# Kernel tuning notes

Measured on AMD Instinct MI355X. Metric: run time of the kernel, lower is better.

Reference implementation:

```python
import jax, jax.numpy as jnp
import numpy as np

N_NODES = 100000
N_EDGES = 1600000
IN_G = 128
IN_R = 64
HID = 128
N_GRAPHS = 512
BN_EPS = 1e-5


def _gcn_conv(x, W, b, src, dst, norm, n_nodes):
    # PyG GCNConv: h = X W; out[i] = sum_j norm_ij * h[j] over edges (incl. self-loops); + bias
    h = x @ W  # [N, C]
    msgs = h[src] * norm[:, None]  # [E', C]
    agg = jax.ops.segment_sum(msgs, dst, num_segments=n_nodes)
    return agg + b


def setup_inputs() -> dict:
    key = jax.random.key(0)
    ks = jax.random.split(key, 12)
    x = jax.random.normal(ks[0], (N_NODES, IN_G), dtype=jnp.float32)
    edge_index = jax.random.randint(ks[1], (2, N_EDGES), 0, N_NODES, dtype=jnp.int64)
    batch = jnp.sort(jax.random.randint(ks[2], (N_NODES,), 0, N_GRAPHS, dtype=jnp.int64))
    rst = jax.random.normal(ks[3], (N_GRAPHS, IN_R), dtype=jnp.float32)

    def lin(k, fan_in, fan_out):
        bound = 1.0 / np.sqrt(fan_in)
        k1, k2 = jax.random.split(k)
        W = jax.random.uniform(k1, (fan_in, fan_out), minval=-bound, maxval=bound, dtype=jnp.float32)
        b = jax.random.uniform(k2, (fan_out,), minval=-bound, maxval=bound, dtype=jnp.float32)
        return W, b

    W1, b1 = lin(ks[4], IN_G, HID)
    W2, b2 = lin(ks[5], HID, HID)
    Wg, bg = lin(ks[6], HID, HID // 2)
    Wr, br = lin(ks[7], IN_R, HID // 2)
    Wc, bc = lin(ks[8], HID, 2)
    gamma = jnp.ones((HID,), dtype=jnp.float32)
    beta = jnp.zeros((HID,), dtype=jnp.float32)
    return {"x": x, "edge_index": edge_index, "batch": batch, "rst": rst,
            "num_graphs": N_GRAPHS,
            "W1": W1, "b1": b1, "gamma": gamma, "beta": beta,
            "W2": W2, "b2": b2, "Wg": Wg, "bg": bg,
            "Wr": Wr, "br": br, "Wc": Wc, "bc": bc}


def reference(x, edge_index, batch, rst, num_graphs,
              W1, b1, gamma, beta, W2, b2, Wg, bg, Wr, br, Wc, bc):
    n = x.shape[0]
    # add self-loops (PyG GCNConv default)
    loop = jnp.arange(n, dtype=edge_index.dtype)
    src = jnp.concatenate([edge_index[0], loop])
    dst = jnp.concatenate([edge_index[1], loop])
    deg = jax.ops.segment_sum(jnp.ones_like(dst, dtype=x.dtype), dst, num_segments=n)
    dinv = jnp.where(deg > 0, jax.lax.rsqrt(deg), 0.0)
    norm = dinv[src] * dinv[dst]  # [E+N]

    h = _gcn_conv(x, W1, b1, src, dst, norm, n)
    # BatchNorm1d with batch statistics (training math; dropout omitted / eval)
    mu = jnp.mean(h, axis=0)
    var = jnp.var(h, axis=0)
    h = gamma * (h - mu) * jax.lax.rsqrt(var + BN_EPS) + beta
    h = jax.nn.relu(h)
    h = _gcn_conv(h, W2, b2, src, dst, norm, n)

    # global mean pool
    sums = jax.ops.segment_sum(h, batch, num_segments=num_graphs)
    counts = jax.ops.segment_sum(jnp.ones((n,), dtype=h.dtype), batch, num_segments=num_graphs)
    pooled = sums / jnp.maximum(counts, 1.0)[:, None]  # [G, HID]

    x_graph = jax.nn.relu(pooled @ Wg + bg)
    x_rst = jax.nn.relu(rst @ Wr + br)
    x_comb = jnp.concatenate([x_graph, x_rst], axis=1)
    return x_comb @ Wc + bc
```

## Files before the change

kernel.cpp:

```cpp
#include <hip/hip_runtime.h>


typedef __attribute__((ext_vector_type(8))) short bf16x8;
typedef __attribute__((ext_vector_type(4))) float f32x4;
typedef __attribute__((ext_vector_type(2))) float f32x2;
typedef __attribute__((ext_vector_type(2))) unsigned u32x2;
typedef __attribute__((ext_vector_type(4))) unsigned u32x4;

#define NBKT_MAX 256
#define BKT_SHIFT 9
#define TILE_E 2000
#define BSORT_CAP 4096

__device__ __forceinline__ float bf_lo(unsigned u) {
  union { unsigned u; float f; } c; c.u = u << 16; return c.f;
}
__device__ __forceinline__ float bf_hi(unsigned u) {
  union { unsigned u; float f; } c; c.u = u & 0xffff0000u; return c.f;
}
__device__ __forceinline__ unsigned short f32_bf16(float f) {
  union { float f; unsigned u; } c; c.f = f;
  return (unsigned short)((c.u + 0x7fffu + ((c.u >> 16) & 1u)) >> 16);
}
__device__ __forceinline__ unsigned pack_bf16(float a, float b) {
  return (unsigned)f32_bf16(a) | ((unsigned)f32_bf16(b) << 16);
}
__device__ __forceinline__ unsigned pack_fp8x4(float c0, float c1, float c2, float c3) {
  int w = __builtin_amdgcn_cvt_pk_fp8_f32(c0, c1, 0, false);
  w = __builtin_amdgcn_cvt_pk_fp8_f32(c2, c3, w, true);
  return (unsigned)w;
}

__global__ __launch_bounds__(256) void tile_hist_kernel(const int* __restrict__ dst,
                                                        int* __restrict__ tcnt,
                                                        int* __restrict__ counts,
                                                        float* __restrict__ stats,
                                                        int e, int ntiles, int nbkt, int n) {
  __shared__ int hist[NBKT_MAX];
  int tile = blockIdx.x, tid = threadIdx.x;
  int idx = blockIdx.x * 256 + tid;
  if (idx < n) counts[idx] = 1;
  if (idx < 256) stats[idx] = 0.f;
  for (int b = tid; b < nbkt; b += 256) hist[b] = 0;
  __syncthreads();
  int t0 = tile * TILE_E;
  int tend = t0 + TILE_E; if (tend > e) tend = e;
  for (int i = t0 + tid; i < tend; i += 256)
    atomicAdd(&hist[__builtin_nontemporal_load(&dst[i]) >> BKT_SHIFT], 1);
  __syncthreads();
  for (int b = tid; b < nbkt; b += 256) tcnt[b * ntiles + tile] = hist[b];
}

__global__ __launch_bounds__(256) void tile_scatter_kernel(const int* __restrict__ src,
                                                           const int* __restrict__ dst,
                                                           const int* __restrict__ tcnt,
                                                           const int* __restrict__ toff,
                                                           int2* __restrict__ pedge,
                                                           int e, int ntiles, int nbkt) {
  __shared__ int hb[NBKT_MAX], cnt[NBKT_MAX], gbase[NBKT_MAX];
  __shared__ int2 led[TILE_E];
  int tile = blockIdx.x, tid = threadIdx.x;
  for (int b = tid; b < nbkt; b += 256) {
    hb[b] = tcnt[b * ntiles + tile];
    gbase[b] = toff[b * ntiles + tile];
    cnt[b] = 0;
  }
  __syncthreads();
  if (tid < 64) {
    int b4 = tid * 4;
    int h0 = (b4 + 0 < nbkt) ? hb[b4 + 0] : 0;
    int h1 = (b4 + 1 < nbkt) ? hb[b4 + 1] : 0;
    int h2 = (b4 + 2 < nbkt) ? hb[b4 + 2] : 0;
    int h3 = (b4 + 3 < nbkt) ? hb[b4 + 3] : 0;
    int local = h0 + h1 + h2 + h3, v = local;
#pragma unroll
    for (int d = 1; d < 64; d <<= 1) {
      int t = __shfl_up(v, d, 64);
      if (tid >= d) v += t;
    }
    int excl = v - local;
    if (b4 + 0 < nbkt) hb[b4 + 0] = excl;
    if (b4 + 1 < nbkt) hb[b4 + 1] = excl + h0;
    if (b4 + 2 < nbkt) hb[b4 + 2] = excl + h0 + h1;
    if (b4 + 3 < nbkt) hb[b4 + 3] = excl + h0 + h1 + h2;
  }
  __syncthreads();
  int t0 = tile * TILE_E;
  int tend = t0 + TILE_E; if (tend > e) tend = e;
  for (int i = t0 + tid; i < tend; i += 256) {
    int s = __builtin_nontemporal_load(&src[i]);
    int d = __builtin_nontemporal_load(&dst[i]);
    int bkt = d >> BKT_SHIFT;
    int slot = hb[bkt] + atomicAdd(&cnt[bkt], 1);
    led[slot] = make_int2(s, d);
  }
  __syncthreads();
  int tc = tend - t0;
  for (int j = tid; j < tc; j += 256) {
    int2 sd = led[j];
    int bkt = sd.y >> BKT_SHIFT;
    pedge[gbase[bkt] + (j - hb[bkt])] = sd;
  }
}

__global__ __launch_bounds__(256) void deg_count_kernel(const int2* __restrict__ pedge,
                                                        const int* __restrict__ toff,
                                                        int* __restrict__ counts,
                                                        int e, int ntiles, int nbkt, int n) {
  __shared__ int cnt[512];
  int b = blockIdx.x >> 2, qu = blockIdx.x & 3;
  int nb0 = b << BKT_SHIFT;
  int nn = n - nb0; if (nn > 512) nn = 512;
  for (int l = threadIdx.x; l < 512; l += 256) cnt[l] = 0;
  __syncthreads();
  int estart = toff[b * ntiles];
  int eend = (b + 1 < nbkt) ? toff[(b + 1) * ntiles] : e;
  int len = eend - estart;
  int qb = estart + (int)((long long)len * qu / 4);
  int qe = estart + (int)((long long)len * (qu + 1) / 4);
  for (int i = qb + threadIdx.x; i < qe; i += 256)
    atomicAdd(&cnt[pedge[i].y - nb0], 1);
  __syncthreads();
  for (int l = threadIdx.x; l < nn; l += 256) {
    int c = cnt[l];
    if (c) atomicAdd(&counts[nb0 + l], c);
  }
}

__global__ __launch_bounds__(1024) void scan1_kernel(const int* __restrict__ counts,
                                                     int* __restrict__ cursor,
                                                     int* __restrict__ bsum,
                                                     float* __restrict__ dinv, int n) {
  __shared__ int wsum[16];
  int tid = threadIdx.x, lane = tid & 63, wid = tid >> 6;
  int idx = blockIdx.x * 1024 + tid;
  int orig = (idx < n) ? counts[idx] : 0;
  if (dinv != nullptr && idx < n) dinv[idx] = rsqrtf((float)orig);
  int v = orig;
#pragma unroll
  for (int d = 1; d < 64; d <<= 1) {
    int t = __shfl_up(v, d, 64);
    if (lane >= d) v += t;
  }
  if (lane == 63) wsum[wid] = v;
  __syncthreads();
  if (wid == 0 && lane < 16) {
    int s = wsum[lane];
#pragma unroll
    for (int d = 1; d < 16; d <<= 1) {
      int t = __shfl_up(s, d, 64);
      if (lane >= d) s += t;
    }
    wsum[lane] = s;
  }
  __syncthreads();
  int wexcl = (wid == 0) ? 0 : wsum[wid - 1];
  if (idx < n) cursor[idx] = wexcl + (v - orig);
  if (tid == 0) bsum[blockIdx.x] = wsum[15];
}

__global__ __launch_bounds__(256) void scan2_kernel(const int* __restrict__ bsum,
                                                    int* __restrict__ boff, int nb) {
  __shared__ int wsum[4];
  int tid = threadIdx.x, lane = tid & 63, wid = tid >> 6;
  int orig = (tid < nb) ? bsum[tid] : 0;
  int v = orig;
#pragma unroll
  for (int d = 1; d < 64; d <<= 1) {
    int t = __shfl_up(v, d, 64);
    if (lane >= d) v += t;
  }
  if (lane == 63) wsum[wid] = v;
  __syncthreads();
  if (tid == 0) {
    int run = 0;
#pragma unroll
    for (int w = 0; w < 4; ++w) { int t = wsum[w]; wsum[w] = run; run += t; }
  }
  __syncthreads();
  if (tid < nb) boff[tid] = wsum[wid] + (v - orig);
}

__global__ void scan3_kernel(int* __restrict__ cursor, const int* __restrict__ boff, int n) {
  int i = blockIdx.x * blockDim.x + threadIdx.x;
  if (i < n) cursor[i] += boff[i >> 10];
}

__global__ __launch_bounds__(256) void bucket_sort_kernel(const int2* __restrict__ pedge,
                                                          const int* __restrict__ toff,
                                                          const int* __restrict__ cursor,
                                                          int* __restrict__ sorted_src,
                                                          int e, int etot,
                                                          int ntiles, int nbkt, int n) {
  __shared__ int lcur[128];
  __shared__ int lsrc[BSORT_CAP];
  int b = blockIdx.x >> 2, qu = blockIdx.x & 3;
  int nb0 = b << BKT_SHIFT;
  int q0 = nb0 + qu * 128;
  if (q0 >= n) return;
  int q1 = q0 + 128; if (q1 > n) q1 = n;
  int qn = q1 - q0;
  int estart = toff[b * ntiles];
  int eend = (b + 1 < nbkt) ? toff[(b + 1) * ntiles] : e;
  int qstart = cursor[q0];
  int qend = (q1 < n) ? cursor[q1] : etot;
  for (int l = threadIdx.x; l < qn; l += 256) lcur[l] = cursor[q0 + l] - qstart;
  __syncthreads();
  for (int i = estart + threadIdx.x; i < eend; i += 256) {
    int2 sd = pedge[i];
    unsigned rel = (unsigned)(sd.y - q0);
    if (rel < (unsigned)qn) {
      int pos = atomicAdd(&lcur[rel], 1);
      if (pos < BSORT_CAP) lsrc[pos] = sd.x;
    }
  }
  __syncthreads();
  for (int l = threadIdx.x; l < qn; l += 256) {
    int pos = lcur[l];
    if (pos < BSORT_CAP) lsrc[pos] = q0 + l;
  }
  __syncthreads();
  int qc = qend - qstart; if (qc > BSORT_CAP) qc = BSORT_CAP;
  for (int j = threadIdx.x; j < qc; j += 256) sorted_src[qstart + j] = lsrc[j];
}

template <int MODE>
__global__ __launch_bounds__(256) void gemm_mfma_kernel(const void* __restrict__ Ap,
                                                        const float* __restrict__ W,
                                                        const float* __restrict__ dinv,
                                                        const float* __restrict__ stats,
                                                        const float* __restrict__ gamma,
                                                        const float* __restrict__ beta,
                                                        unsigned* __restrict__ Cb, int n) {
  __shared__ unsigned short WB[16384];
  __shared__ float scs[128], shs[128];
  int tid = threadIdx.x;
  if (MODE == 1 && tid < 128) {
    float invN = 1.f / (float)n;
    float mu = stats[tid] * invN;
    float var = stats[128 + tid] * invN - mu * mu;
    float rstd = rsqrtf(var + 1e-5f);
    float s = gamma[tid] * rstd;
    scs[tid] = s;
    shs[tid] = beta[tid] - mu * s;
  }
  for (int t = tid; t < 2048; t += 256) {
    int nl = t & 15, ct = (t >> 4) & 7, qq = (t >> 7) & 3, kt = t >> 9;
    int c = ct * 16 + nl;
    int k0 = kt * 32 + qq * 8;
    union { bf16x8 v; unsigned short s[8]; } u;
#pragma unroll
    for (int j = 0; j < 8; ++j) u.s[j] = f32_bf16(W[(k0 + j) * 128 + c]);
    *(bf16x8*)&WB[(size_t)t * 8] = u.v;
  }
  __syncthreads();
  int lane = tid & 63;
  int m = lane & 15, q = lane >> 4;
  float scr[4][8], shr[4][8];
  if (MODE == 1) {
#pragma unroll
    for (int kt = 0; kt < 4; ++kt)
#pragma unroll
      for (int j = 0; j < 8; ++j) {
        int c = kt * 32 + q * 8 + j;
        scr[kt][j] = scs[c];
        shr[kt][j] = shs[c];
      }
  }
  int wv = (int)((blockIdx.x * 256u + tid) >> 6);
  int nwv = (int)((gridDim.x * 256u) >> 6);
  int ntl = n >> 4;
  for (int t = wv; t < ntl; t += nwv) {
    int row = t * 16 + m;
    bf16x8 af[4];
    if (MODE == 1) {
      const u32x4* Au = (const u32x4*)((const unsigned*)Ap + (size_t)row * 64 + q * 4);
#pragma unroll
      for (int kt = 0; kt < 4; ++kt) {
        u32x4 w = Au[kt * 4];
        float y0 = fmaxf(fmaf(scr[kt][0], bf_lo(w.x), shr[kt][0]), 0.f);
        float y1 = fmaxf(fmaf(scr[kt][1], bf_hi(w.x), shr[kt][1]), 0.f);
        float y2 = fmaxf(fmaf(scr[kt][2], bf_lo(w.y), shr[kt][2]), 0.f);
        float y3 = fmaxf(fmaf(scr[kt][3], bf_hi(w.y), shr[kt][3]), 0.f);
        float y4 = fmaxf(fmaf(scr[kt][4], bf_lo(w.z), shr[kt][4]), 0.f);
        float y5 = fmaxf(fmaf(scr[kt][5], bf_hi(w.z), shr[kt][5]), 0.f);
        float y6 = fmaxf(fmaf(scr[kt][6], bf_lo(w.w), shr[kt][6]), 0.f);
        float y7 = fmaxf(fmaf(scr[kt][7], bf_hi(w.w), shr[kt][7]), 0.f);
        union { bf16x8 v; unsigned uu[4]; } uf;
        uf.uu[0] = pack_bf16(y0, y1);
        uf.uu[1] = pack_bf16(y2, y3);
        uf.uu[2] = pack_bf16(y4, y5);
        uf.uu[3] = pack_bf16(y6, y7);
        af[kt] = uf.v;
      }
    } else {
      const float* Arow = (const float*)Ap + (size_t)row * 128 + q * 8;
#pragma unroll
      for (int kt = 0; kt < 4; ++kt) {
        f32x4 a0 = *(const f32x4*)(Arow + kt * 32);
        f32x4 a1 = *(const f32x4*)(Arow + kt * 32 + 4);
        union { bf16x8 v; unsigned short s[8]; } u;
        u.s[0] = f32_bf16(a0.x); u.s[1] = f32_bf16(a0.y);
        u.s[2] = f32_bf16(a0.z); u.s[3] = f32_bf16(a0.w);
        u.s[4] = f32_bf16(a1.x); u.s[5] = f32_bf16(a1.y);
        u.s[6] = f32_bf16(a1.z); u.s[7] = f32_bf16(a1.w);
        af[kt] = u.v;
      }
    }
    f32x4 acc[8];
#pragma unroll
    for (int ct = 0; ct < 8; ++ct) acc[ct] = (f32x4){0.f, 0.f, 0.f, 0.f};
#pragma unroll
    for (int kt = 0; kt < 4; ++kt) {
#pragma unroll
      for (int ct = 0; ct < 8; ++ct) {
        bf16x8 b = *(const bf16x8*)&WB[(((kt * 4 + q) * 8 + ct) * 16 + m) * 8];
        acc[ct] = __builtin_amdgcn_mfma_f32_16x16x32_bf16(b, af[kt], acc[ct], 0, 0, 0);
      }
    }
    float dv = dinv[row];
#pragma unroll
    for (int ct = 0; ct < 8; ++ct) {
      unsigned wout = pack_fp8x4(acc[ct][0] * dv, acc[ct][1] * dv,
                                 acc[ct][2] * dv, acc[ct][3] * dv);
      Cb[(size_t)row * 32 + ct * 4 + q] = wout;
    }
  }
}

__global__ __launch_bounds__(256) void gather_kernel(const unsigned* __restrict__ g,
    const int* __restrict__ srcs, const int* __restrict__ cursor,
    const int* __restrict__ counts, const float* __restrict__ dinv,
    unsigned* __restrict__ out, int n) {
  int lane = threadIdx.x & 63;
  int grp = lane >> 4;
  int sub = lane & 15;
  int gw = (int)((blockIdx.x * blockDim.x + threadIdx.x) >> 6);
  int nw = (int)((gridDim.x * blockDim.x) >> 6);
  for (int i0 = gw; i0 < n; i0 += nw) {
    int i = __builtin_amdgcn_readfirstlane(i0);
    int beg = cursor[i];
    int cnt2 = counts[i];
    float di = dinv[i];
    f32x2 A0 = {0.f, 0.f}, A1 = {0.f, 0.f}, A2 = {0.f, 0.f}, A3 = {0.f, 0.f};
#define ACC8(W0, W1)                                                       \
    { A0 += __builtin_amdgcn_cvt_pk_f32_fp8((int)(W0), false);             \
      A1 += __builtin_amdgcn_cvt_pk_f32_fp8((int)(W0), true);              \
      A2 += __builtin_amdgcn_cvt_pk_f32_fp8((int)(W1), false);             \
      A3 += __builtin_amdgcn_cvt_pk_f32_fp8((int)(W1), true); }
    int e = 0;
    for (; e + 16 <= cnt2; e += 16) {
      int sA = srcs[beg + e + grp];
      int sB = srcs[beg + e + grp + 4];
      int sC = srcs[beg + e + grp + 8];
      int sD = srcs[beg + e + grp + 12];
      u32x2 vA = *((const u32x2*)(g + ((size_t)sA << 5)) + sub);
      u32x2 vB = *((const u32x2*)(g + ((size_t)sB << 5)) + sub);
      u32x2 vC = *((const u32x2*)(g + ((size_t)sC << 5)) + sub);
      u32x2 vD = *((const u32x2*)(g + ((size_t)sD << 5)) + sub);
      ACC8(vA.x, vA.y) ACC8(vB.x, vB.y) ACC8(vC.x, vC.y) ACC8(vD.x, vD.y)
    }
    for (; e + 4 <= cnt2; e += 4) {
      int s = srcs[beg + e + grp];
      u32x2 v = *((const u32x2*)(g + ((size_t)s << 5)) + sub);
      ACC8(v.x, v.y)
    }
    if (e < cnt2) {
      int k = e + grp;
      int kk = (k < cnt2) ? k : cnt2 - 1;
      int s = srcs[beg + kk];
      float sel = (k < cnt2) ? 1.f : 0.f;
      u32x2 v = *((const u32x2*)(g + ((size_t)s << 5)) + sub);
      f32x2 p0 = __builtin_amdgcn_cvt_pk_f32_fp8((int)v.x, false);
      f32x2 p1 = __builtin_amdgcn_cvt_pk_f32_fp8((int)v.x, true);
      f32x2 p2 = __builtin_amdgcn_cvt_pk_f32_fp8((int)v.y, false);
      f32x2 p3 = __builtin_amdgcn_cvt_pk_f32_fp8((int)v.y, true);
      A0 += p0 * sel; A1 += p1 * sel; A2 += p2 * sel; A3 += p3 * sel;
    }
#undef ACC8
    float a0 = A0.x, a1 = A0.y, a2 = A1.x, a3 = A1.y;
    float a4 = A2.x, a5 = A2.y, a6 = A3.x, a7 = A3.y;
    a0 += __shfl_xor(a0, 16, 64); a0 += __shfl_xor(a0, 32, 64);
    a1 += __shfl_xor(a1, 16, 64); a1 += __shfl_xor(a1, 32, 64);
    a2 += __shfl_xor(a2, 16, 64); a2 += __shfl_xor(a2, 32, 64);
    a3 += __shfl_xor(a3, 16, 64); a3 += __shfl_xor(a3, 32, 64);
    a4 += __shfl_xor(a4, 16, 64); a4 += __shfl_xor(a4, 32, 64);
    a5 += __shfl_xor(a5, 16, 64); a5 += __shfl_xor(a5, 32, 64);
    a6 += __shfl_xor(a6, 16, 64); a6 += __shfl_xor(a6, 32, 64);
    a7 += __shfl_xor(a7, 16, 64); a7 += __shfl_xor(a7, 32, 64);
    if (grp == 0) {
      u32x4 o;
      o.x = pack_bf16(di * a0, di * a1);
      o.y = pack_bf16(di * a2, di * a3);
      o.z = pack_bf16(di * a4, di * a5);
      o.w = pack_bf16(di * a6, di * a7);
      *((u32x4*)(out + ((size_t)i << 6)) + sub) = o;
    }
  }
}

__global__ __launch_bounds__(256) void bn_stats_kernel(const unsigned* __restrict__ a,
                                                       float* __restrict__ stats, int n) {
  int c2 = threadIdx.x & 63;
  int ph = threadIdx.x >> 6;
  float s0 = 0.f, s1 = 0.f, q0 = 0.f, q1 = 0.f;
  for (int r = blockIdx.x * 4 + ph; r < n; r += gridDim.x * 4) {
    unsigned v = a[(size_t)r * 64 + c2];
    float x0 = bf_lo(v), x1 = bf_hi(v);
    s0 += x0; s1 += x1; q0 += x0 * x0; q1 += x1 * x1;
  }
  __shared__ float ls[4][64][4];
  ls[ph][c2][0] = s0; ls[ph][c2][1] = s1; ls[ph][c2][2] = q0; ls[ph][c2][3] = q1;
  __syncthreads();
  if (threadIdx.x < 64) {
    int c = threadIdx.x;
    float S0 = 0.f, S1 = 0.f, Q0 = 0.f, Q1 = 0.f;
#pragma unroll
    for (int p = 0; p < 4; ++p) {
      S0 += ls[p][c][0]; S1 += ls[p][c][1]; Q0 += ls[p][c][2]; Q1 += ls[p][c][3];
    }
    atomicAdd(&stats[2 * c], S0);
    atomicAdd(&stats[2 * c + 1], S1);
    atomicAdd(&stats[128 + 2 * c], Q0);
    atomicAdd(&stats[129 + 2 * c], Q1);
  }
}

__global__ void gstart_kernel(const int* __restrict__ batch, int* __restrict__ gstart,
                              int n, int G) {
  int g = blockIdx.x * blockDim.x + threadIdx.x;
  if (g > G) return;
  if (g == G) { gstart[g] = n; return; }
  int lo = 0, hi = n;
  while (lo < hi) {
    int mid = (lo + hi) >> 1;
    if (batch[mid] < g) lo = mid + 1; else hi = mid;
  }
  gstart[g] = lo;
}

__global__ __launch_bounds__(256) void pool_kernel(const unsigned* __restrict__ a,
    const int* __restrict__ gstart, const float* __restrict__ b2,
    float* __restrict__ pooled, int G) {
  int g = blockIdx.x;
  int c2 = threadIdx.x & 63;
  int ph = threadIdx.x >> 6;
  int s = gstart[g], e = gstart[g + 1];
  float a0 = 0.f, a1 = 0.f;
  for (int r = s + ph; r < e; r += 4) {
    unsigned v = a[(size_t)r * 64 + c2];
    a0 += bf_lo(v); a1 += bf_hi(v);
  }
  __shared__ float ls[4][64][2];
  ls[ph][c2][0] = a0; ls[ph][c2][1] = a1;
  __syncthreads();
  if (threadIdx.x < 64) {
    int c = threadIdx.x;
    float S0 = 0.f, S1 = 0.f;
#pragma unroll
    for (int p = 0; p < 4; ++p) { S0 += ls[p][c][0]; S1 += ls[p][c][1]; }
    int cnt = e - s;
    float inv = (cnt > 0) ? 1.f / (float)cnt : 0.f;
    float2 res;
    res.x = (cnt > 0) ? (S0 * inv + b2[2 * c]) : 0.f;
    res.y = (cnt > 0) ? (S1 * inv + b2[2 * c + 1]) : 0.f;
    ((float2*)(pooled + (size_t)g * 128))[c] = res;
  }
}

__global__ __launch_bounds__(128) void head_kernel(const float* __restrict__ pooled,
    const float* __restrict__ rst, const float* __restrict__ Wg, const float* __restrict__ bg,
    const float* __restrict__ Wr, const float* __restrict__ br, const float* __restrict__ Wc,
    const float* __restrict__ bc, float* __restrict__ out, int G) {
  int g = blockIdx.x;
  int t = threadIdx.x;
  __shared__ float xc[128];
  if (t < 64) {
    float acc = bg[t];
    const float* __restrict__ p = pooled + (size_t)g * 128;
    for (int k = 0; k < 128; ++k) acc = fmaf(p[k], Wg[k * 64 + t], acc);
    xc[t] = fmaxf(acc, 0.f);
  } else {
    int j = t - 64;
    float acc = br[j];
    const float* __restrict__ r = rst + (size_t)g * 64;
    for (int k = 0; k < 64; ++k) acc = fmaf(r[k], Wr[k * 64 + j], acc);
    xc[t] = fmaxf(acc, 0.f);
  }
  __syncthreads();
  if (t < 2) {
    float acc = bc[t];
    for (int j = 0; j < 128; ++j) acc = fmaf(xc[j], Wc[j * 2 + t], acc);
    out[(size_t)g * 2 + t] = acc;
  }
}

extern "C" void kernel_launch(void* const* d_in, const int* in_sizes, int n_in,
                              void* d_out, int out_size, void* d_ws, size_t ws_size,
                              hipStream_t stream) {
  (void)n_in; (void)ws_size;
  const float* x     = (const float*)d_in[0];
  const int*   ei    = (const int*)d_in[1];
  const int*   batch = (const int*)d_in[2];
  const float* rst   = (const float*)d_in[3];
  const float* W1    = (const float*)d_in[5];
  const float* gamma = (const float*)d_in[7];
  const float* beta  = (const float*)d_in[8];
  const float* W2    = (const float*)d_in[9];
  const float* b2    = (const float*)d_in[10];
  const float* Wg    = (const float*)d_in[11];
  const float* bg    = (const float*)d_in[12];
  const float* Wr    = (const float*)d_in[13];
  const float* br    = (const float*)d_in[14];
  const float* Wc    = (const float*)d_in[15];
  const float* bc    = (const float*)d_in[16];
  float* out = (float*)d_out;

  int N = in_sizes[0] / 128;
  int E = in_sizes[1] / 2;
  int G = out_size / 2;
  int ETOT = E + N;
  const int* esrc = ei;
  const int* edst = ei + E;

  int nbkt = (N + 511) >> BKT_SHIFT;
  int ntiles = (E + TILE_E - 1) / TILE_E;
  int tlen = nbkt * ntiles;

  char* ws = (char*)d_ws;
  size_t off = 0;
  auto alloc = [&](size_t bytes) -> void* {
    void* p = ws + off;
    off += (bytes + 255) & ~(size_t)255;
    return p;
  };
  unsigned* hb  = (unsigned*)alloc((size_t)N * 32 * 4);
  unsigned* agb = (unsigned*)alloc((size_t)N * 64 * 4);
  int* sorted   = (int*)alloc((size_t)ETOT * 4 + 256);
  int2* pedge   = (int2*)alloc((size_t)E * 8);
  int* tcnt     = (int*)alloc((size_t)tlen * 4);
  int* toff     = (int*)alloc((size_t)tlen * 4);
  int* counts   = (int*)alloc((size_t)N * 4);
  int* cursor   = (int*)alloc((size_t)N * 4);
  float* dinv   = (float*)alloc((size_t)N * 4);
  float* stats  = (float*)alloc(256 * 4);
  int* gstart   = (int*)alloc((size_t)(G + 1) * 4);
  float* pooled = (float*)alloc((size_t)G * 128 * 4);
  int* bsum     = (int*)alloc(256 * 4);
  int* boff     = (int*)alloc(256 * 4);
  int* tbsum    = (int*)alloc(256 * 4);
  int* tboff    = (int*)alloc(256 * 4);

  int nscan = (N + 1023) / 1024;
  int ntscan = (tlen + 1023) / 1024;

  tile_hist_kernel<<<ntiles, 256, 0, stream>>>(edst, tcnt, counts, stats, E, ntiles, nbkt, N);
  scan1_kernel<<<ntscan, 1024, 0, stream>>>(tcnt, toff, tbsum, nullptr, tlen);
  scan2_kernel<<<1, 256, 0, stream>>>(tbsum, tboff, ntscan);
  scan3_kernel<<<(tlen + 255) / 256, 256, 0, stream>>>(toff, tboff, tlen);
  tile_scatter_kernel<<<ntiles, 256, 0, stream>>>(esrc, edst, tcnt, toff, pedge, E, ntiles, nbkt);
  deg_count_kernel<<<nbkt * 4, 256, 0, stream>>>(pedge, toff, counts, E, ntiles, nbkt, N);
  scan1_kernel<<<nscan, 1024, 0, stream>>>(counts, cursor, bsum, dinv, N);
  scan2_kernel<<<1, 256, 0, stream>>>(bsum, boff, nscan);
  scan3_kernel<<<(N + 255) / 256, 256, 0, stream>>>(cursor, boff, N);
  bucket_sort_kernel<<<nbkt * 4, 256, 0, stream>>>(pedge, toff, cursor, sorted,
                                                   E, ETOT, ntiles, nbkt, N);

  gemm_mfma_kernel<0><<<1024, 256, 0, stream>>>(x, W1, dinv, stats, gamma, beta, hb, N);
  gather_kernel<<<4096, 256, 0, stream>>>(hb, sorted, cursor, counts, dinv, agb, N);

  bn_stats_kernel<<<512, 256, 0, stream>>>(agb, stats, N);

  gemm_mfma_kernel<1><<<1024, 256, 0, stream>>>(agb, W2, dinv, stats, gamma, beta, hb, N);
  gather_kernel<<<4096, 256, 0, stream>>>(hb, sorted, cursor, counts, dinv, agb, N);

  gstart_kernel<<<(G + 1 + 255) / 256, 256, 0, stream>>>(batch, gstart, N, G);
  pool_kernel<<<G, 256, 0, stream>>>(agb, gstart, b2, pooled, G);
  head_kernel<<<G, 128, 0, stream>>>(pooled, rst, Wg, bg, Wr, br, Wc, bc, out, G);
}
```

Baseline: 369.2 us.

## Cut kernel launches: single-pass ticket scans, fused pool+head, gstart into hist

Replaces the three-kernel scan (block scan, block-sum scan, add-back) with one kernel. The last-arriving block, chosen by an atomic ticket, scans the block sums while every other block spin-waits on a flag. It also folds the graph-start binary search into the histogram kernel, fuses mean pooling with the MLP head, and resizes the GEMM grid to match the node count. The goal is to remove several small launches and their inter-kernel gaps. The spin-wait depends on all blocks being resident at once, which holds for these small scan grids but would be fragile for larger ones.

After: 375.6 us. No clear change (+1.7%).

```diff
diff --git a/kernel.cpp b/kernel.cpp
--- a/kernel.cpp
+++ b/kernel.cpp
@@ -30,17 +30,35 @@
   w = __builtin_amdgcn_cvt_pk_fp8_f32(c2, c3, w, true);
   return (unsigned)w;
 }
+__device__ __forceinline__ int aload(int* p) { return atomicAdd(p, 0); }
 
 __global__ __launch_bounds__(256) void tile_hist_kernel(const int* __restrict__ dst,
                                                         int* __restrict__ tcnt,
                                                         int* __restrict__ counts,
                                                         float* __restrict__ stats,
-                                                        int e, int ntiles, int nbkt, int n) {
+                                                        const int* __restrict__ batch,
+                                                        int* __restrict__ gstart,
+                                                        int* __restrict__ syncp,
+                                                        int e, int ntiles, int nbkt,
+                                                        int n, int G) {
   __shared__ int hist[NBKT_MAX];
   int tile = blockIdx.x, tid = threadIdx.x;
   int idx = blockIdx.x * 256 + tid;
   if (idx < n) counts[idx] = 1;
   if (idx < 256) stats[idx] = 0.f;
+  if (idx < 8) syncp[idx] = 0;
+  if (idx <= G) {
+    int g = idx;
+    if (g == G) gstart[g] = n;
+    else {
+      int lo = 0, hi = n;
+      while (lo < hi) {
+        int mid = (lo + hi) >> 1;
+        if (batch[mid] < g) lo = mid + 1; else hi = mid;
+      }
+      gstart[g] = lo;
+    }
+  }
   for (int b = tid; b < nbkt; b += 256) hist[b] = 0;
   __syncthreads();
   int t0 = tile * TILE_E;
@@ -49,6 +67,78 @@
     atomicAdd(&hist[__builtin_nontemporal_load(&dst[i]) >> BKT_SHIFT], 1);
   __syncthreads();
   for (int b = tid; b < nbkt; b += 256) tcnt[b * ntiles + tile] = hist[b];
+}
+
+__global__ __launch_bounds__(1024) void scan_ticket_kernel(const int* __restrict__ src,
+                                                           int* __restrict__ dst,
+                                                           int* __restrict__ bsum,
+                                                           int* __restrict__ boff,
+                                                           int* __restrict__ syncp,
+                                                           float* __restrict__ dinv,
+                                                           int n, int nb) {
+  __shared__ int wsum[16];
+  __shared__ int sflag, soff;
+  int tid = threadIdx.x, lane = tid & 63, wid = tid >> 6;
+  int bid = blockIdx.x;
+  int idx = bid * 1024 + tid;
+  int orig = (idx < n) ? src[idx] : 0;
+  if (dinv != nullptr && idx < n) dinv[idx] = rsqrtf((float)orig);
+  int v = orig;
+#pragma unroll
+  for (int d = 1; d < 64; d <<= 1) {
+    int t = __shfl_up(v, d, 64);
+    if (lane >= d) v += t;
+  }
+  if (lane == 63) wsum[wid] = v;
+  __syncthreads();
+  if (wid == 0 && lane < 16) {
+    int s = wsum[lane];
+#pragma unroll
+    for (int d = 1; d < 16; d <<= 1) {
+      int t = __shfl_up(s, d, 64);
+      if (lane >= d) s += t;
+    }
+    wsum[lane] = s;
+  }
+  __syncthreads();
+  int wexcl = (wid == 0) ? 0 : wsum[wid - 1];
+  int lexcl = wexcl + (v - orig);
+  if (tid == 0) {
+    atomicExch(&bsum[bid], wsum[15]);
+    __threadfence();
+    int t = atomicAdd(&syncp[0], 1);
+    sflag = (t == nb - 1) ? 1 : 0;
+  }
+  __syncthreads();
+  if (sflag) {
+    if (tid < 64) {
+      int base = tid * 4;
+      int a0 = (base + 0 < nb) ? aload(&bsum[base + 0]) : 0;
+      int a1 = (base + 1 < nb) ? aload(&bsum[base + 1]) : 0;
+      int a2 = (base + 2 < nb) ? aload(&bsum[base + 2]) : 0;
+      int a3 = (base + 3 < nb) ? aload(&bsum[base + 3]) : 0;
+      int local = a0 + a1 + a2 + a3, s = local;
+#pragma unroll
+      for (int d = 1; d < 64; d <<= 1) {
+        int t = __shfl_up(s, d, 64);
+        if (tid >= d) s += t;
+      }
+      int excl = s - local;
+      if (base + 0 < nb) atomicExch(&boff[base + 0], excl);
+      if (base + 1 < nb) atomicExch(&boff[base + 1], excl + a0);
+      if (base + 2 < nb) atomicExch(&boff[base + 2], excl + a0 + a1);
+      if (base + 3 < nb) atomicExch(&boff[base + 3], excl + a0 + a1 + a2);
+      __threadfence();
+    }
+    __syncthreads();
+    if (tid == 0) atomicExch(&syncp[1], 1);
+  }
+  if (tid == 0) {
+    while (aload(&syncp[1]) == 0) __builtin_amdgcn_s_sleep(8);
+    soff = aload(&boff[bid]);
+  }
+  __syncthreads();
+  if (idx < n) dst[idx] = soff + lexcl;
 }
 
 __global__ __launch_bounds__(256) void tile_scatter_kernel(const int* __restrict__ src,
@@ -125,65 +215,6 @@
     int c = cnt[l];
     if (c) atomicAdd(&counts[nb0 + l], c);
   }
-}
-
-__global__ __launch_bounds__(1024) void scan1_kernel(const int* __restrict__ counts,
-                                                     int* __restrict__ cursor,
-                                                     int* __restrict__ bsum,
-                                                     float* __restrict__ dinv, int n) {
-  __shared__ int wsum[16];
-  int tid = threadIdx.x, lane = tid & 63, wid = tid >> 6;
-  int idx = blockIdx.x * 1024 + tid;
-  int orig = (idx < n) ? counts[idx] : 0;
-  if (dinv != nullptr && idx < n) dinv[idx] = rsqrtf((float)orig);
-  int v = orig;
-#pragma unroll
-  for (int d = 1; d < 64; d <<= 1) {
-    int t = __shfl_up(v, d, 64);
-    if (lane >= d) v += t;
-  }
-  if (lane == 63) wsum[wid] = v;
-  __syncthreads();
-  if (wid == 0 && lane < 16) {
-    int s = wsum[lane];
-#pragma unroll
-    for (int d = 1; d < 16; d <<= 1) {
-      int t = __shfl_up(s, d, 64);
-      if (lane >= d) s += t;
-    }
-    wsum[lane] = s;
-  }
-  __syncthreads();
-  int wexcl = (wid == 0) ? 0 : wsum[wid - 1];
-  if (idx < n) cursor[idx] = wexcl + (v - orig);
-  if (tid == 0) bsum[blockIdx.x] = wsum[15];
-}
-
-__global__ __launch_bounds__(256) void scan2_kernel(const int* __restrict__ bsum,
-                                                    int* __restrict__ boff, int nb) {
-  __shared__ int wsum[4];
-  int tid = threadIdx.x, lane = tid & 63, wid = tid >> 6;
-  int orig = (tid < nb) ? bsum[tid] : 0;
-  int v = orig;
-#pragma unroll
-  for (int d = 1; d < 64; d <<= 1) {
-    int t = __shfl_up(v, d, 64);
-    if (lane >= d) v += t;
-  }
-  if (lane == 63) wsum[wid] = v;
-  __syncthreads();
-  if (tid == 0) {
-    int run = 0;
-#pragma unroll
-    for (int w = 0; w < 4; ++w) { int t = wsum[w]; wsum[w] = run; run += t; }
-  }
-  __syncthreads();
-  if (tid < nb) boff[tid] = wsum[wid] + (v - orig);
-}
-
-__global__ void scan3_kernel(int* __restrict__ cursor, const int* __restrict__ boff, int n) {
-  int i = blockIdx.x * blockDim.x + threadIdx.x;
-  if (i < n) cursor[i] += boff[i >> 10];
 }
 
 __global__ __launch_bounds__(256) void bucket_sort_kernel(const int2* __restrict__ pedge,
@@ -426,25 +457,16 @@
   }
 }
 
-__global__ void gstart_kernel(const int* __restrict__ batch, int* __restrict__ gstart,
-                              int n, int G) {
-  int g = blockIdx.x * blockDim.x + threadIdx.x;
-  if (g > G) return;
-  if (g == G) { gstart[g] = n; return; }
-  int lo = 0, hi = n;
-  while (lo < hi) {
-    int mid = (lo + hi) >> 1;
-    if (batch[mid] < g) lo = mid + 1; else hi = mid;
-  }
-  gstart[g] = lo;
-}
-
-__global__ __launch_bounds__(256) void pool_kernel(const unsigned* __restrict__ a,
+__global__ __launch_bounds__(256) void poolhead_kernel(const unsigned* __restrict__ a,
     const int* __restrict__ gstart, const float* __restrict__ b2,
-    float* __restrict__ pooled, int G) {
+    const float* __restrict__ rst, const float* __restrict__ Wg,
+    const float* __restrict__ bg, const float* __restrict__ Wr,
+    const float* __restrict__ br, const float* __restrict__ Wc,
+    const float* __restrict__ bc, float* __restrict__ out, int G) {
   int g = blockIdx.x;
-  int c2 = threadIdx.x & 63;
-  int ph = threadIdx.x >> 6;
+  int t = threadIdx.x;
+  int c2 = t & 63;
+  int ph = t >> 6;
   int s = gstart[g], e = gstart[g + 1];
   float a0 = 0.f, a1 = 0.f;
   for (int r = s + ph; r < e; r += 4) {
@@ -452,35 +474,26 @@
     a0 += bf_lo(v); a1 += bf_hi(v);
   }
   __shared__ float ls[4][64][2];
+  __shared__ float xp[128];
+  __shared__ float xc[128];
   ls[ph][c2][0] = a0; ls[ph][c2][1] = a1;
   __syncthreads();
-  if (threadIdx.x < 64) {
-    int c = threadIdx.x;
+  if (t < 64) {
+    int c = t;
     float S0 = 0.f, S1 = 0.f;
 #pragma unroll
     for (int p = 0; p < 4; ++p) { S0 += ls[p][c][0]; S1 += ls[p][c][1]; }
     int cnt = e - s;
     float inv = (cnt > 0) ? 1.f / (float)cnt : 0.f;
-    float2 res;
-    res.x = (cnt > 0) ? (S0 * inv + b2[2 * c]) : 0.f;
-    res.y = (cnt > 0) ? (S1 * inv + b2[2 * c + 1]) : 0.f;
-    ((float2*)(pooled + (size_t)g * 128))[c] = res;
-  }
-}
-
-__global__ __launch_bounds__(128) void head_kernel(const float* __restrict__ pooled,
-    const float* __restrict__ rst, const float* __restrict__ Wg, const float* __restrict__ bg,
-    const float* __restrict__ Wr, const float* __restrict__ br, const float* __restrict__ Wc,
-    const float* __restrict__ bc, float* __restrict__ out, int G) {
-  int g = blockIdx.x;
-  int t = threadIdx.x;
-  __shared__ float xc[128];
+    xp[2 * c]     = (cnt > 0) ? (S0 * inv + b2[2 * c]) : 0.f;
+    xp[2 * c + 1] = (cnt > 0) ? (S1 * inv + b2[2 * c + 1]) : 0.f;
+  }
+  __syncthreads();
   if (t < 64) {
     float acc = bg[t];
-    const float* __restrict__ p = pooled + (size_t)g * 128;
-    for (int k = 0; k < 128; ++k) acc = fmaf(p[k], Wg[k * 64 + t], acc);
+    for (int k = 0; k < 128; ++k) acc = fmaf(xp[k], Wg[k * 64 + t], acc);
     xc[t] = fmaxf(acc, 0.f);
-  } else {
+  } else if (t < 128) {
     int j = t - 64;
     float acc = br[j];
     const float* __restrict__ r = rst + (size_t)g * 64;
@@ -545,36 +558,33 @@
   float* dinv   = (float*)alloc((size_t)N * 4);
   float* stats  = (float*)alloc(256 * 4);
   int* gstart   = (int*)alloc((size_t)(G + 1) * 4);
-  float* pooled = (float*)alloc((size_t)G * 128 * 4);
   int* bsum     = (int*)alloc(256 * 4);
   int* boff     = (int*)alloc(256 * 4);
-  int* tbsum    = (int*)alloc(256 * 4);
-  int* tboff    = (int*)alloc(256 * 4);
+  int* syncp    = (int*)alloc(8 * 4);
 
   int nscan = (N + 1023) / 1024;
   int ntscan = (tlen + 1023) / 1024;
-
-  tile_hist_kernel<<<ntiles, 256, 0, stream>>>(edst, tcnt, counts, stats, E, ntiles, nbkt, N);
-  scan1_kernel<<<ntscan, 1024, 0, stream>>>(tcnt, toff, tbsum, nullptr, tlen);
-  scan2_kernel<<<1, 256, 0, stream>>>(tbsum, tboff, ntscan);
-  scan3_kernel<<<(tlen + 255) / 256, 256, 0, stream>>>(toff, tboff, tlen);
+  int gblocks = (N / 16 + 3) / 4;
+
+  tile_hist_kernel<<<ntiles, 256, 0, stream>>>(edst, tcnt, counts, stats, batch,
+                                               gstart, syncp, E, ntiles, nbkt, N, G);
+  scan_ticket_kernel<<<ntscan, 1024, 0, stream>>>(tcnt, toff, bsum, boff,
+                                                  syncp, nullptr, tlen, ntscan);
   tile_scatter_kernel<<<ntiles, 256, 0, stream>>>(esrc, edst, tcnt, toff, pedge, E, ntiles, nbkt);
   deg_count_kernel<<<nbkt * 4, 256, 0, stream>>>(pedge, toff, counts, E, ntiles, nbkt, N);
-  scan1_kernel<<<nscan, 1024, 0, stream>>>(counts, cursor, bsum, dinv, N);
-  scan2_kernel<<<1, 256, 0, stream>>>(bsum, boff, nscan);
-  scan3_kernel<<<(N + 255) / 256, 256, 0, stream>>>(cursor, boff, N);
+  scan_ticket_kernel<<<nscan, 1024, 0, stream>>>(counts, cursor, bsum, boff,
+                                                 syncp + 2, dinv, N, nscan);
   bucket_sort_kernel<<<nbkt * 4, 256, 0, stream>>>(pedge, toff, cursor, sorted,
                                                    E, ETOT, ntiles, nbkt, N);
 
-  gemm_mfma_kernel<0><<<1024, 256, 0, stream>>>(x, W1, dinv, stats, gamma, beta, hb, N);
+  gemm_mfma_kernel<0><<<gblocks, 256, 0, stream>>>(x, W1, dinv, stats, gamma, beta, hb, N);
   gather_kernel<<<4096, 256, 0, stream>>>(hb, sorted, cursor, counts, dinv, agb, N);
 
   bn_stats_kernel<<<512, 256, 0, stream>>>(agb, stats, N);
 
-  gemm_mfma_kernel<1><<<1024, 256, 0, stream>>>(agb, W2, dinv, stats, gamma, beta, hb, N);
+  gemm_mfma_kernel<1><<<gblocks, 256, 0, stream>>>(agb, W2, dinv, stats, gamma, beta, hb, N);
   gather_kernel<<<4096, 256, 0, stream>>>(hb, sorted, cursor, counts, dinv, agb, N);
 
-  gstart_kernel<<<(G + 1 + 255) / 256, 256, 0, stream>>>(batch, gstart, N, G);
-  pool_kernel<<<G, 256, 0, stream>>>(agb, gstart, b2, pooled, G);
-  head_kernel<<<G, 128, 0, stream>>>(pooled, rst, Wg, bg, Wr, br, Wc, bc, out, G);
-}
+  poolhead_kernel<<<G, 256, 0, stream>>>(agb, gstart, b2, rst, Wg, bg, Wr, br,
+                                         Wc, bc, out, G);
+}
```
